# Optimization experiments

Hardware: AMD Instinct MI355X
Metric: run time of the kernel (lower is better)

Reference implementation:

```python
import jax, jax.numpy as jnp
import numpy as np

# Mamba2 derived dims (headdim=64, ngroups=1, mamba_ssm defaults)
D_MODEL = 1024
D_STATE = 64
D_CONV = 4
EXPAND = 2
D_INNER = EXPAND * D_MODEL          # 2048
HEADDIM = 64
NHEADS = D_INNER // HEADDIM          # 32
CONV_DIM = D_INNER + 2 * D_STATE     # 2176 (x, B, C share the depthwise conv)
D_IN_PROJ = 2 * D_INNER + 2 * D_STATE + NHEADS  # 4256 (z, xBC, dt)
BATCH, SEQ = 8, 1024


def setup_inputs() -> dict:
    key = jax.random.key(0)
    ks = jax.random.split(key, 8)
    g = lambda k, shp, sc=0.02: (jax.random.normal(k, shp, jnp.float32) * sc)
    # dt_bias init as in mamba_ssm: inverse-softplus of dt ~ U[1e-3, 1e-1] (log-uniform)
    dt = jnp.exp(jax.random.uniform(ks[3], (NHEADS,), jnp.float32)
                 * (jnp.log(0.1) - jnp.log(0.001)) + jnp.log(0.001))
    dt_bias = dt + jnp.log(-jnp.expm1(-dt))  # softplus^{-1}(dt)
    A_log = jnp.log(jax.random.uniform(ks[4], (NHEADS,), jnp.float32, 1.0, 16.0))
    return {
        "x": jax.random.normal(ks[0], (BATCH, SEQ, D_MODEL), jnp.float32),
        "W_in": g(ks[1], (D_MODEL, D_IN_PROJ)),
        "conv_w": g(ks[2], (D_CONV, CONV_DIM), 0.2),
        "conv_b": jnp.zeros((CONV_DIM,), jnp.float32),
        "dt_bias": dt_bias,
        "A_log": A_log,
        "Dskip": jnp.ones((NHEADS,), jnp.float32),
        "norm_w": jnp.ones((D_INNER,), jnp.float32),
        "W_out": g(ks[5], (D_INNER, D_MODEL)),
        "head_w": g(ks[6], (D_MODEL, 1)),
        "head_b": jnp.zeros((1,), jnp.float32),
    }


def _mamba2(x, W_in, conv_w, conv_b, dt_bias, A_log, Dskip, norm_w, W_out):
    b, l, _ = x.shape
    zxbcdt = x @ W_in                                   # (b, l, 4256)
    z = zxbcdt[..., :D_INNER]
    xBC = zxbcdt[..., D_INNER:D_INNER + CONV_DIM]
    dt = jax.nn.softplus(zxbcdt[..., D_INNER + CONV_DIM:] + dt_bias)  # (b, l, h)
    # causal depthwise conv1d (kernel D_CONV) + SiLU
    pad = jnp.pad(xBC, ((0, 0), (D_CONV - 1, 0), (0, 0)))
    conv = conv_b + sum(pad[:, k:k + l, :] * conv_w[k] for k in range(D_CONV))
    xBC = jax.nn.silu(conv)
    xh = xBC[..., :D_INNER].reshape(b, l, NHEADS, HEADDIM)
    B = xBC[..., D_INNER:D_INNER + D_STATE]             # (b, l, s) ngroups=1
    C = xBC[..., D_INNER + D_STATE:]                    # (b, l, s)
    A = -jnp.exp(A_log)                                 # (h,)
    dA = jnp.exp(dt * A)                                # (b, l, h)

    def step(h, inps):
        dA_t, dt_t, B_t, C_t, x_t = inps                # (b,h),(b,h),(b,s),(b,s),(b,h,p)
        h = h * dA_t[:, :, None, None] + (dt_t[:, :, None] * x_t)[..., None] * B_t[:, None, None, :]
        y = jnp.einsum('bhps,bs->bhp', h, C_t)
        return h, y

    tm = lambda a: jnp.moveaxis(a, 1, 0)                # time-major for scan
    h0 = jnp.zeros((b, NHEADS, HEADDIM, D_STATE), x.dtype)
    _, y = jax.lax.scan(step, h0, (tm(dA), tm(dt), tm(B), tm(C), tm(xh)))
    y = jnp.moveaxis(y, 0, 1) + Dskip[None, None, :, None] * xh   # skip connection
    # gated RMSNorm: norm(y * silu(z)) * weight
    y = y.reshape(b, l, D_INNER) * jax.nn.silu(z)
    y = y * jax.lax.rsqrt(jnp.mean(y * y, axis=-1, keepdims=True) + 1e-5) * norm_w
    return y @ W_out                                    # (b, l, d_model)


def reference(x, W_in, conv_w, conv_b, dt_bias, A_log, Dskip, norm_w, W_out, head_w, head_b):
    y = _mamba2(x, W_in, conv_w, conv_b, dt_bias, A_log, Dskip, norm_w, W_out)
    return y @ head_w + head_b                          # (b, l, 1)
```

## Files before the change

### kernel.cpp

```cpp
#include <hip/hip_runtime.h>
#include <hip/hip_bf16.h>

#define D_MODEL   1024
#define D_STATE   64
#define D_INNER   2048
#define NHEADS    32
#define CONV_DIM  2176
#define D_IN_PROJ 4256
#define NPAD      4352
#define BATCH     8
#define SEQ       1024
#define NROWS     8192
#define NCHUNK    8
#define CLEN      128

typedef __attribute__((ext_vector_type(8))) short bf16x8;
typedef __attribute__((ext_vector_type(4))) float f32x4;

__device__ __forceinline__ float bf2f(unsigned short u){
  unsigned v = ((unsigned)u) << 16;
  return __builtin_bit_cast(float, v);
}
__device__ __forceinline__ unsigned short f2bf(float f){
  __hip_bfloat16 h = __float2bfloat16(f);
  return __builtin_bit_cast(unsigned short, h);
}

__global__ __launch_bounds__(256) void k_convert_x(const float* __restrict__ x,
                                                   unsigned short* __restrict__ xb){
  int i = blockIdx.x*256 + threadIdx.x;
  float4 v = ((const float4*)x)[i];
  ushort4 o;
  o.x = f2bf(v.x); o.y = f2bf(v.y); o.z = f2bf(v.z); o.w = f2bf(v.w);
  ((ushort4*)xb)[i] = o;
}

__global__ __launch_bounds__(256) void k_transpose_win(const float* __restrict__ W_in,
                                                       unsigned short* __restrict__ wt){
  __shared__ float tile[32][33];
  int n0 = blockIdx.x * 32;
  int k0 = blockIdx.y * 32;
  int tx = threadIdx.x & 31;
  int ty = threadIdx.x >> 5;
  #pragma unroll
  for (int i = 0; i < 4; ++i){
    int kk = ty + i*8;
    int n  = n0 + tx;
    tile[kk][tx] = (n < D_IN_PROJ) ? W_in[(size_t)(k0+kk)*D_IN_PROJ + n] : 0.f;
  }
  __syncthreads();
  #pragma unroll
  for (int i = 0; i < 4; ++i){
    int nn = ty + i*8;
    wt[(size_t)(n0+nn)*D_MODEL + k0 + tx] = f2bf(tile[tx][nn]);
  }
}

__global__ __launch_bounds__(256) void k_nwc(const float* __restrict__ W_out,
                                             const float* __restrict__ head_w,
                                             const float* __restrict__ norm_w,
                                             float* __restrict__ nwc){
  int d    = blockIdx.x*4 + (threadIdx.x >> 6);
  int lane = threadIdx.x & 63;
  const float* row = W_out + (size_t)d * D_MODEL;
  float s = 0.f;
  #pragma unroll
  for (int k = lane; k < D_MODEL; k += 64) s += row[k] * head_w[k];
  #pragma unroll
  for (int off = 32; off; off >>= 1) s += __shfl_down(s, off);
  if (lane == 0) nwc[d] = s * norm_w[d];
}

__global__ __launch_bounds__(512, 1) void k_gemm256(const unsigned short* __restrict__ A,
                                                    const unsigned short* __restrict__ BT,
                                                    unsigned short* __restrict__ C){
  __shared__ unsigned short smem[65536];
  int bid  = blockIdx.x;
  int m0   = (bid / 17) << 8;
  int n0   = (bid % 17) << 8;
  int tid  = threadIdx.x;
  int w    = tid >> 6, lane = tid & 63;
  int wr   = w >> 2, wc = w & 3;
  int stR  = tid >> 3;
  int stC  = (tid & 7) << 3;
  int wb   = w << 9;

  f32x4 acc[8][4];
  #pragma unroll
  for (int i = 0; i < 8; ++i)
    #pragma unroll
    for (int j = 0; j < 4; ++j) acc[i][j] = (f32x4){0.f,0.f,0.f,0.f};

  const unsigned short* sA0 = A  + (size_t)(m0 + stR)*D_MODEL + stC;
  const unsigned short* sB0 = BT + (size_t)(n0 + stR)*D_MODEL + stC;

#define STAGE256(bb, kt) { \
    const unsigned short* pa = sA0 + (size_t)(kt)*64; \
    const unsigned short* pb = sB0 + (size_t)(kt)*64; \
    _Pragma("unroll") \
    for (int it = 0; it < 4; ++it){ \
      __builtin_amdgcn_global_load_lds((const __attribute__((address_space(1))) void*)(pa + (size_t)it*64*D_MODEL), \
          (__attribute__((address_space(3))) void*)(smem + (bb)*32768 + it*4096 + wb), 16, 0, 0); \
      __builtin_amdgcn_global_load_lds((const __attribute__((address_space(1))) void*)(pb + (size_t)it*64*D_MODEL), \
          (__attribute__((address_space(3))) void*)(smem + (bb)*32768 + 16384 + it*4096 + wb), 16, 0, 0); \
    } }

  STAGE256(0, 0);

  int frow = lane & 15, fk = (lane >> 4) << 3;

  for (int t = 0; t < 16; ++t){
    int cur = t & 1;
    asm volatile("" ::: "memory");
    __builtin_amdgcn_s_barrier();
    if (t < 15){
      STAGE256(cur ^ 1, t + 1);
      asm volatile("s_waitcnt vmcnt(8)" ::: "memory");
    } else {
      asm volatile("s_waitcnt vmcnt(0)" ::: "memory");
    }
    __builtin_amdgcn_s_barrier();
    asm volatile("" ::: "memory");

    const unsigned short* At = smem + cur*32768;
    const unsigned short* Bt = At + 16384;
    __builtin_amdgcn_s_setprio(1);
    #pragma unroll
    for (int kk = 0; kk < 64; kk += 32){
      bf16x8 af[8], bfr[4];
      #pragma unroll
      for (int mf = 0; mf < 8; ++mf)
        af[mf] = *(const bf16x8*)(At + (wr*128 + mf*16 + frow)*64 + kk + fk);
      #pragma unroll
      for (int nf = 0; nf < 4; ++nf)
        bfr[nf] = *(const bf16x8*)(Bt + (wc*64 + nf*16 + frow)*64 + kk + fk);
      #pragma unroll
      for (int mf = 0; mf < 8; ++mf)
        #pragma unroll
        for (int nf = 0; nf < 4; ++nf)
          acc[mf][nf] = __builtin_amdgcn_mfma_f32_16x16x32_bf16(af[mf], bfr[nf], acc[mf][nf], 0, 0, 0);
    }
    __builtin_amdgcn_s_setprio(0);
  }
#undef STAGE256

  int crow = (lane >> 4) << 2, ccol = lane & 15;
  #pragma unroll
  for (int mf = 0; mf < 8; ++mf)
    #pragma unroll
    for (int nf = 0; nf < 4; ++nf){
      size_t base = (size_t)(m0 + wr*128 + mf*16 + crow)*NPAD + (n0 + wc*64 + nf*16 + ccol);
      #pragma unroll
      for (int r = 0; r < 4; ++r)
        C[base + (size_t)r*NPAD] = f2bf(acc[mf][nf][r]);
    }
}

__global__ __launch_bounds__(256) void k_dtda(const unsigned short* __restrict__ zx,
                                              const float* __restrict__ dt_bias,
                                              float* __restrict__ dtb){
  int i = blockIdx.x*256 + threadIdx.x;
  int r = i >> 5, h = i & 31;
  float raw = bf2f(zx[(size_t)r*NPAD + D_INNER + CONV_DIM + h]) + dt_bias[h];
  float dt  = (raw > 20.f) ? raw : log1pf(expf(raw));
  int b = r >> 10, l = r & 1023;
  dtb[(b*32 + h)*1024 + l] = dt;
}

__global__ __launch_bounds__(256) void k_conv(const unsigned short* __restrict__ zx,
                                              const float* __restrict__ conv_w,
                                              const float* __restrict__ conv_b,
                                              unsigned short* __restrict__ xbc,
                                              unsigned short* __restrict__ bc16){
  int r = blockIdx.x;
  int l = r & (SEQ - 1);
  for (int oc = threadIdx.x; oc < 272; oc += 256){
    int c = oc * 8;
    float acc[8];
    #pragma unroll
    for (int j = 0; j < 8; ++j) acc[j] = conv_b[c + j];
    #pragma unroll
    for (int k = 0; k < 4; ++k){
      int dl = l + k - 3;
      if (dl >= 0){
        bf16x8 v = *(const bf16x8*)(zx + (size_t)(r + k - 3)*NPAD + D_INNER + c);
        #pragma unroll
        for (int j = 0; j < 8; ++j)
          acc[j] = fmaf(bf2f((unsigned short)v[j]), conv_w[k*CONV_DIM + c + j], acc[j]);
      }
    }
    bf16x8 o;
    #pragma unroll
    for (int j = 0; j < 8; ++j){
      float s = acc[j] / (1.f + expf(-acc[j]));
      o[j] = (short)f2bf(s);
    }
    if (c < D_INNER) *(bf16x8*)(xbc  + (size_t)r*D_INNER + c) = o;
    else             *(bf16x8*)(bc16 + (size_t)r*128 + (c - D_INNER)) = o;
  }
}

__global__ __launch_bounds__(64) void k_cs(const float* __restrict__ dtb,
                                           const float* __restrict__ A_log,
                                           float* __restrict__ csb,
                                           float* __restrict__ cumA){
  int id = blockIdx.x;
  int bh = id >> 3, c = id & 7;
  int h  = bh & 31;
  int l  = threadIdx.x;
  const float* src = dtb + (size_t)bh*1024 + (c << 7);
  float d0 = src[2*l], d1 = src[2*l + 1];
  float pr = d0 + d1;
  float s  = pr;
  #pragma unroll
  for (int off = 1; off < 64; off <<= 1){
    float n = __shfl_up(s, off);
    if (l >= off) s += n;
  }
  float excl = s - pr;
  csb[(size_t)id*128 + 2*l]     = excl + d0;
  csb[(size_t)id*128 + 2*l + 1] = excl + pr;
  if (l == 63){
    float A = -expf(A_log[h]);
    cumA[id] = expf(A * s);
  }
}

__global__ __launch_bounds__(256) void k_ssd1(const unsigned short* __restrict__ xbc,
                                              const unsigned short* __restrict__ bc16,
                                              const float* __restrict__ dtb,
                                              const float* __restrict__ csb,
                                              const float* __restrict__ A_log,
                                              unsigned short* __restrict__ hend){
  __shared__ __align__(16) unsigned short XTw[64*136];
  __shared__ __align__(16) unsigned short BTl[64*136];
  int id = blockIdx.x;
  int bh = id >> 3, c = id & 7;
  int b  = bh >> 5, h = bh & 31;
  int tid = threadIdx.x;
  int w = tid >> 6, l = tid & 63;
  float A = -expf(A_log[h]);
  int row0 = b*SEQ + (c << 7);
  float csT = csb[(size_t)id*128 + 127];

  #pragma unroll
  for (int it = 0; it < 4; ++it){
    int idx = it*256 + tid;
    int tau = idx >> 3, pb = idx & 7;
    bf16x8 v = *(const bf16x8*)(xbc + (size_t)(row0+tau)*D_INNER + h*64 + pb*8);
    float wgt = dtb[(size_t)bh*1024 + (c<<7) + tau]
              * expf(A*(csT - csb[(size_t)id*128 + tau]));
    #pragma unroll
    for (int j = 0; j < 8; ++j)
      XTw[(pb*8+j)*136 + tau] = f2bf(bf2f((unsigned short)v[j]) * wgt);
  }
  #pragma unroll
  for (int it = 0; it < 4; ++it){
    int idx = it*256 + tid;
    int tau = idx >> 3, sb = idx & 7;
    bf16x8 v = *(const bf16x8*)(bc16 + (size_t)(row0+tau)*128 + sb*8);
    #pragma unroll
    for (int j = 0; j < 8; ++j)
      BTl[(sb*8+j)*136 + tau] = (unsigned short)v[j];
  }
  __syncthreads();

  int fr = l & 15, fo = (l >> 4) << 3;
  f32x4 acc[4];
  #pragma unroll
  for (int n = 0; n < 4; ++n) acc[n] = (f32x4){0.f,0.f,0.f,0.f};
  #pragma unroll
  for (int kt = 0; kt < 4; ++kt){
    bf16x8 pf = *(const bf16x8*)(XTw + (w*16+fr)*136 + kt*32 + fo);
    #pragma unroll
    for (int n = 0; n < 4; ++n){
      bf16x8 qf = *(const bf16x8*)(BTl + (n*16+fr)*136 + kt*32 + fo);
      acc[n] = __builtin_amdgcn_mfma_f32_16x16x32_bf16(pf, qf, acc[n], 0, 0, 0);
    }
  }
  #pragma unroll
  for (int n = 0; n < 4; ++n)
    #pragma unroll
    for (int r = 0; r < 4; ++r){
      int p = w*16 + ((l>>4)<<2) + r;
      int s = n*16 + fr;
      hend[(size_t)id*4096 + p*64 + s] = f2bf(acc[n][r]);
    }
}

__global__ __launch_bounds__(256) void k_comb(unsigned short* __restrict__ hh,
                                              const float* __restrict__ cumA){
  int bh = blockIdx.x, tid = threadIdx.x;
  float carry[16];
  #pragma unroll
  for (int i = 0; i < 16; ++i) carry[i] = 0.f;
  #pragma unroll
  for (int c = 0; c < NCHUNK; ++c){
    size_t base = (((size_t)bh*NCHUNK + c) << 12) + tid*16;
    bf16x8 a0 = *(const bf16x8*)(hh + base);
    bf16x8 a1 = *(const bf16x8*)(hh + base + 8);
    float ca = cumA[bh*NCHUNK + c];
    float tmp[16];
    #pragma unroll
    for (int i = 0; i < 8; ++i){
      tmp[i]   = bf2f((unsigned short)a0[i]);
      tmp[8+i] = bf2f((unsigned short)a1[i]);
    }
    bf16x8 w0, w1;
    #pragma unroll
    for (int i = 0; i < 8; ++i){
      w0[i] = (short)f2bf(carry[i]);
      w1[i] = (short)f2bf(carry[8+i]);
    }
    *(bf16x8*)(hh + base)     = w0;
    *(bf16x8*)(hh + base + 8) = w1;
    #pragma unroll
    for (int i = 0; i < 16; ++i) carry[i] = tmp[i] + ca*carry[i];
  }
}

__global__ __launch_bounds__(256, 2) void k_ssd2(const unsigned short* __restrict__ xbc,
                                                 const unsigned short* __restrict__ bc16,
                                                 const unsigned short* __restrict__ zx,
                                                 const float* __restrict__ dtb,
                                                 const float* __restrict__ csb,
                                                 const float* __restrict__ A_log,
                                                 const float* __restrict__ Dskip,
                                                 const unsigned short* __restrict__ hbuf,
                                                 unsigned short* __restrict__ yb){
  __shared__ __align__(16) unsigned short Cl[128*72];
  __shared__ __align__(16) unsigned short XTl[64*136];
  __shared__ __align__(16) unsigned short Gm[128*136];
  __shared__ float cs_l[128], dt_l[128], a_l[128];

  int id = blockIdx.x;
  int bh = id >> 3, c = id & 7;
  int b  = bh >> 5, h = bh & 31;
  int tid = threadIdx.x;
  int w = tid >> 6, l = tid & 63;
  float A = -expf(A_log[h]);
  int row0 = b*SEQ + (c << 7);

  #pragma unroll
  for (int it = 0; it < 4; ++it){
    int idx = it*256 + tid;
    int tau = idx >> 3, cb = idx & 7;
    bf16x8 v = *(const bf16x8*)(bc16 + (size_t)(row0+tau)*128 + 64 + cb*8);
    *(bf16x8*)(Cl + tau*72 + cb*8) = v;
  }
  #pragma unroll
  for (int it = 0; it < 4; ++it){
    int idx = it*256 + tid;
    int tau = idx >> 3, pb = idx & 7;
    bf16x8 v = *(const bf16x8*)(xbc + (size_t)(row0+tau)*D_INNER + h*64 + pb*8);
    #pragma unroll
    for (int j = 0; j < 8; ++j)
      XTl[(pb*8+j)*136 + tau] = (unsigned short)v[j];
  }
  if (tid < 128){
    float cs = csb[(size_t)id*128 + tid];
    cs_l[tid] = cs;
    dt_l[tid] = dtb[(size_t)bh*1024 + (c<<7) + tid];
    a_l[tid]  = expf(A*cs);
  }
  __syncthreads();

  int fr = l & 15, fo = (l >> 4) << 3;
  int mtB = 7 - w;

  f32x4 Y[2][4];
  #pragma unroll
  for (int mi = 0; mi < 2; ++mi)
    #pragma unroll
    for (int n = 0; n < 4; ++n) Y[mi][n] = (f32x4){0.f,0.f,0.f,0.f};
  #pragma unroll
  for (int mi = 0; mi < 2; ++mi){
    int mt = mi ? mtB : w;
    #pragma unroll
    for (int kt = 0; kt < 2; ++kt){
      bf16x8 pf = *(const bf16x8*)(Cl + (mt*16+fr)*72 + kt*32 + fo);
      #pragma unroll
      for (int n = 0; n < 4; ++n){
        bf16x8 qf = *(const bf16x8*)(hbuf + (size_t)id*4096 + (n*16+fr)*64 + kt*32 + fo);
        Y[mi][n] = __builtin_amdgcn_mfma_f32_16x16x32_bf16(pf, qf, Y[mi][n], 0, 0, 0);
      }
    }
    #pragma unroll
    for (int r = 0; r < 4; ++r){
      float av = a_l[mt*16 + ((l>>4)<<2) + r];
      #pragma unroll
      for (int n = 0; n < 4; ++n) Y[mi][n][r] *= av;
    }
  }

  f32x4 Sv[9];
  #pragma unroll
  for (int slot = 0; slot < 9; ++slot){
    int mt = (slot <= w) ? w : mtB;
    int nt = (slot <= w) ? slot : slot - w - 1;
    f32x4 acc = (f32x4){0.f,0.f,0.f,0.f};
    #pragma unroll
    for (int kt = 0; kt < 2; ++kt){
      bf16x8 pf = *(const bf16x8*)(Cl + (mt*16+fr)*72 + kt*32 + fo);
      bf16x8 qf = *(const bf16x8*)(bc16 + (size_t)(row0 + nt*16+fr)*128 + kt*32 + fo);
      acc = __builtin_amdgcn_mfma_f32_16x16x32_bf16(pf, qf, acc, 0, 0, 0);
    }
    int tau = nt*16 + fr;
    float dtt = dt_l[tau];
    float cst = cs_l[tau];
    #pragma unroll
    for (int r = 0; r < 4; ++r){
      int t = mt*16 + ((l>>4)<<2) + r;
      float v = acc[r] * dtt * expf(A*(cs_l[t] - cst));
      acc[r] = (tau <= t) ? v : 0.f;
    }
    Sv[slot] = acc;
  }

  #pragma unroll
  for (int slot = 0; slot < 9; ++slot){
    int mt = (slot <= w) ? w : mtB;
    int nt = (slot <= w) ? slot : slot - w - 1;
    int tau = nt*16 + fr;
    #pragma unroll
    for (int r = 0; r < 4; ++r){
      int t = mt*16 + ((l>>4)<<2) + r;
      Gm[t*136 + tau] = f2bf(Sv[slot][r]);
    }
  }
  {
    int mtE = (w & 1) ? mtB : w;
    int ntE = mtE + 1;
    #pragma unroll
    for (int r = 0; r < 4; ++r){
      int t = mtE*16 + ((l>>4)<<2) + r;
      Gm[t*136 + ntE*16 + fr] = 0;
    }
  }
  __syncthreads();

  #pragma unroll
  for (int mi = 0; mi < 2; ++mi){
    int mt = mi ? mtB : w;
    int kmax = (mt + 2) >> 1;
    for (int kt2 = 0; kt2 < kmax; ++kt2){
      bf16x8 pf = *(const bf16x8*)(Gm + (mt*16+fr)*136 + kt2*32 + fo);
      #pragma unroll
      for (int n = 0; n < 4; ++n){
        bf16x8 qf = *(const bf16x8*)(XTl + (n*16+fr)*136 + kt2*32 + fo);
        Y[mi][n] = __builtin_amdgcn_mfma_f32_16x16x32_bf16(pf, qf, Y[mi][n], 0, 0, 0);
      }
    }
  }

  float dsk = Dskip[h];
  #pragma unroll
  for (int mi = 0; mi < 2; ++mi){
    int mt = mi ? mtB : w;
    #pragma unroll
    for (int r = 0; r < 4; ++r){
      int t = mt*16 + ((l>>4)<<2) + r;
      size_t orow = (size_t)(row0 + t)*D_INNER + h*64;
      size_t zrow = (size_t)(row0 + t)*NPAD + h*64;
      #pragma unroll
      for (int n = 0; n < 4; ++n){
        int p = n*16 + fr;
        float xv = bf2f(XTl[p*136 + t]);
        float zf = bf2f(zx[zrow + p]);
        float yv = Y[mi][n][r] + dsk*xv;
        float g  = yv * (zf / (1.f + expf(-zf)));
        yb[orow + p] = f2bf(g);
      }
    }
  }
}

__global__ __launch_bounds__(256) void k_epilogue(const unsigned short* __restrict__ yg,
                                                  const float* __restrict__ nwc,
                                                  const float* __restrict__ head_b,
                                                  float* __restrict__ out){
  int r   = blockIdx.x;
  int tid = threadIdx.x;
  bf16x8 y8 = *(const bf16x8*)(yg + (size_t)r*D_INNER + tid*8);
  float4 w0 = ((const float4*)nwc)[tid*2];
  float4 w1 = ((const float4*)nwc)[tid*2 + 1];
  float wv[8] = {w0.x, w0.y, w0.z, w0.w, w1.x, w1.y, w1.z, w1.w};
  float s2 = 0.f, sd = 0.f;
  #pragma unroll
  for (int k = 0; k < 8; ++k){
    float g = bf2f((unsigned short)y8[k]);
    s2 += g*g; sd += g*wv[k];
  }
  #pragma unroll
  for (int off = 32; off; off >>= 1){
    s2 += __shfl_down(s2, off);
    sd += __shfl_down(sd, off);
  }
  __shared__ float r2[4], rd[4];
  if ((tid & 63) == 0){ r2[tid >> 6] = s2; rd[tid >> 6] = sd; }
  __syncthreads();
  if (tid == 0){
    float t2 = r2[0] + r2[1] + r2[2] + r2[3];
    float td = rd[0] + rd[1] + rd[2] + rd[3];
    out[r] = rsqrtf(t2 * (1.f/2048.f) + 1e-5f) * td + head_b[0];
  }
}

extern "C" void kernel_launch(void* const* d_in, const int* in_sizes, int n_in,
                              void* d_out, int out_size, void* d_ws, size_t ws_size,
                              hipStream_t stream){
  const float* x       = (const float*)d_in[0];
  const float* W_in    = (const float*)d_in[1];
  const float* conv_w  = (const float*)d_in[2];
  const float* conv_b  = (const float*)d_in[3];
  const float* dt_bias = (const float*)d_in[4];
  const float* A_log   = (const float*)d_in[5];
  const float* Dskip   = (const float*)d_in[6];
  const float* norm_w  = (const float*)d_in[7];
  const float* W_out   = (const float*)d_in[8];
  const float* head_w  = (const float*)d_in[9];
  const float* head_b  = (const float*)d_in[10];
  float* out = (float*)d_out;

  char* ws = (char*)d_ws;
  unsigned short* xb   = (unsigned short*)(ws + 0);
  unsigned short* wt   = (unsigned short*)(ws + 16777216);
  unsigned short* zx16 = (unsigned short*)(ws + 25690112);
  unsigned short* xbc  = (unsigned short*)(ws + 96993280);
  float*          dtb  = (float*)         (ws + 132644864);
  float*          nwc  = (float*)         (ws + 134742016);
  unsigned short* yb   = (unsigned short*)(ws + 134750208);

  unsigned short* hbuf = xb;
  unsigned short* bc16 = wt;
  float*          csb  = (float*)(ws + 16777216 + 2097152);
  float*          cumA = (float*)(ws + 16777216 + 3145728);

  k_convert_x<<<8192, 256, 0, stream>>>(x, xb);
  k_transpose_win<<<dim3(136, 32), 256, 0, stream>>>(W_in, wt);
  k_nwc<<<512, 256, 0, stream>>>(W_out, head_w, norm_w, nwc);
  k_gemm256<<<(NROWS/256)*(NPAD/256), 512, 0, stream>>>(xb, wt, zx16);
  k_dtda<<<1024, 256, 0, stream>>>(zx16, dt_bias, dtb);
  k_conv<<<NROWS, 256, 0, stream>>>(zx16, conv_w, conv_b, xbc, bc16);
  k_cs<<<2048, 64, 0, stream>>>(dtb, A_log, csb, cumA);
  k_ssd1<<<2048, 256, 0, stream>>>(xbc, bc16, dtb, csb, A_log, hbuf);
  k_comb<<<256, 256, 0, stream>>>(hbuf, cumA);
  k_ssd2<<<2048, 256, 0, stream>>>(xbc, bc16, zx16, dtb, csb, A_log, Dskip, hbuf, yb);
  k_epilogue<<<NROWS, 256, 0, stream>>>(yb, nwc, head_b, out);
}
```

Baseline: 274.4 us.

## XOR-swizzle LDS tiles and interleave global-to-LDS loads with MFMA phases

The in-projection GEMM now XOR-swizzles the k-column placement of each row in LDS, applied on the global source address and undone on fragment reads, to cut LDS bank conflicts. The main loop is split into four sub-phases, and the next tile's B and A global_load_lds issues are spread between them with finer vmcnt waits and barriers. The aim is to overlap memory traffic with MFMA work rather than staging a whole tile up front. The risks are a hand-tuned vmcnt and barrier ordering that must exactly match when each buffer region is read, plus extra barriers per iteration.

```diff
diff --git a/kernel.cpp b/kernel.cpp
--- a/kernel.cpp
+++ b/kernel.cpp
@@ -82,8 +82,9 @@
   int w    = tid >> 6, lane = tid & 63;
   int wr   = w >> 2, wc = w & 3;
   int stR  = tid >> 3;
-  int stC  = (tid & 7) << 3;
+  int stCs = (((tid & 7) ^ ((tid >> 3) & 7)) << 3);
   int wb   = w << 9;
+  int frow = lane & 15, fk = (lane >> 4) << 3;
 
   f32x4 acc[8][4];
   #pragma unroll
@@ -91,58 +92,126 @@
     #pragma unroll
     for (int j = 0; j < 4; ++j) acc[i][j] = (f32x4){0.f,0.f,0.f,0.f};
 
-  const unsigned short* sA0 = A  + (size_t)(m0 + stR)*D_MODEL + stC;
-  const unsigned short* sB0 = BT + (size_t)(n0 + stR)*D_MODEL + stC;
-
-#define STAGE256(bb, kt) { \
-    const unsigned short* pa = sA0 + (size_t)(kt)*64; \
-    const unsigned short* pb = sB0 + (size_t)(kt)*64; \
-    _Pragma("unroll") \
-    for (int it = 0; it < 4; ++it){ \
-      __builtin_amdgcn_global_load_lds((const __attribute__((address_space(1))) void*)(pa + (size_t)it*64*D_MODEL), \
-          (__attribute__((address_space(3))) void*)(smem + (bb)*32768 + it*4096 + wb), 16, 0, 0); \
-      __builtin_amdgcn_global_load_lds((const __attribute__((address_space(1))) void*)(pb + (size_t)it*64*D_MODEL), \
-          (__attribute__((address_space(3))) void*)(smem + (bb)*32768 + 16384 + it*4096 + wb), 16, 0, 0); \
-    } }
-
-  STAGE256(0, 0);
-
-  int frow = lane & 15, fk = (lane >> 4) << 3;
+  const unsigned short* sA0 = A  + (size_t)(m0 + stR)*D_MODEL + stCs;
+  const unsigned short* sB0 = BT + (size_t)(n0 + stR)*D_MODEL + stCs;
+
+#define GLD(dstOff, src) __builtin_amdgcn_global_load_lds( \
+    (const __attribute__((address_space(1))) void*)(src), \
+    (__attribute__((address_space(3))) void*)(smem + (dstOff) + wb), 16, 0, 0)
+#define ISSA(bb,kt,i) GLD((bb)*32768 + (i)*4096, \
+    sA0 + (size_t)(kt)*64 + (size_t)(i)*64*D_MODEL)
+#define ISSB(bb,kt,i) GLD((bb)*32768 + 16384 + (i)*4096, \
+    sB0 + (size_t)(kt)*64 + (size_t)(i)*64*D_MODEL)
+#define RD8(base, r, col) (*(const bf16x8*)((base) + (r)*64 + ((col) ^ (((r)&7)<<3))))
+
+  ISSB(0,0,0); ISSB(0,0,1); ISSB(0,0,2); ISSB(0,0,3);
+  ISSA(0,0,0); ISSA(0,0,2); ISSA(0,0,1); ISSA(0,0,3);
+  asm volatile("s_waitcnt vmcnt(2)" ::: "memory");
+  __builtin_amdgcn_s_barrier();
+  asm volatile("" ::: "memory");
 
   for (int t = 0; t < 16; ++t){
-    int cur = t & 1;
-    asm volatile("" ::: "memory");
-    __builtin_amdgcn_s_barrier();
-    if (t < 15){
-      STAGE256(cur ^ 1, t + 1);
-      asm volatile("s_waitcnt vmcnt(8)" ::: "memory");
-    } else {
-      asm volatile("s_waitcnt vmcnt(0)" ::: "memory");
-    }
+    int cur = t & 1, nxt = cur ^ 1;
+    bool iss = (t < 15);
+    const unsigned short* At = smem + cur*32768;
+    const unsigned short* Bt = At + 16384;
+
+    bf16x8 bF[4][2];
+    if (iss){ ISSB(nxt, t+1, 0); ISSB(nxt, t+1, 1); }
+    #pragma unroll
+    for (int nf = 0; nf < 4; ++nf){
+      int r = wc*64 + nf*16 + frow;
+      bF[nf][0] = RD8(Bt, r, fk);
+      bF[nf][1] = RD8(Bt, r, 32 + fk);
+    }
+    {
+      bf16x8 aF[2][2];
+      #pragma unroll
+      for (int mi = 0; mi < 2; ++mi){
+        int r = wr*128 + mi*16 + frow;
+        aF[mi][0] = RD8(At, r, fk);
+        aF[mi][1] = RD8(At, r, 32 + fk);
+      }
+      __builtin_amdgcn_s_setprio(1);
+      #pragma unroll
+      for (int mi = 0; mi < 2; ++mi)
+        #pragma unroll
+        for (int nf = 0; nf < 4; ++nf)
+          #pragma unroll
+          for (int kki = 0; kki < 2; ++kki)
+            acc[mi][nf] = __builtin_amdgcn_mfma_f32_16x16x32_bf16(aF[mi][kki], bF[nf][kki], acc[mi][nf], 0, 0, 0);
+      __builtin_amdgcn_s_setprio(0);
+    }
+    if (iss){ ISSB(nxt, t+1, 2); ISSB(nxt, t+1, 3); }
+    {
+      bf16x8 aF[2][2];
+      #pragma unroll
+      for (int mi = 0; mi < 2; ++mi){
+        int r = wr*128 + (2 + mi)*16 + frow;
+        aF[mi][0] = RD8(At, r, fk);
+        aF[mi][1] = RD8(At, r, 32 + fk);
+      }
+      __builtin_amdgcn_s_setprio(1);
+      #pragma unroll
+      for (int mi = 0; mi < 2; ++mi)
+        #pragma unroll
+        for (int nf = 0; nf < 4; ++nf)
+          #pragma unroll
+          for (int kki = 0; kki < 2; ++kki)
+            acc[2 + mi][nf] = __builtin_amdgcn_mfma_f32_16x16x32_bf16(aF[mi][kki], bF[nf][kki], acc[2 + mi][nf], 0, 0, 0);
+      __builtin_amdgcn_s_setprio(0);
+    }
+    if (iss) asm volatile("s_waitcnt vmcnt(4)" ::: "memory");
+    else     asm volatile("s_waitcnt vmcnt(0)" ::: "memory");
     __builtin_amdgcn_s_barrier();
     asm volatile("" ::: "memory");
-
-    const unsigned short* At = smem + cur*32768;
-    const unsigned short* Bt = At + 16384;
-    __builtin_amdgcn_s_setprio(1);
-    #pragma unroll
-    for (int kk = 0; kk < 64; kk += 32){
-      bf16x8 af[8], bfr[4];
-      #pragma unroll
-      for (int mf = 0; mf < 8; ++mf)
-        af[mf] = *(const bf16x8*)(At + (wr*128 + mf*16 + frow)*64 + kk + fk);
-      #pragma unroll
-      for (int nf = 0; nf < 4; ++nf)
-        bfr[nf] = *(const bf16x8*)(Bt + (wc*64 + nf*16 + frow)*64 + kk + fk);
-      #pragma unroll
-      for (int mf = 0; mf < 8; ++mf)
+    if (iss){ ISSA(nxt, t+1, 0); ISSA(nxt, t+1, 2); }
+    {
+      bf16x8 aF[2][2];
+      #pragma unroll
+      for (int mi = 0; mi < 2; ++mi){
+        int r = wr*128 + (4 + mi)*16 + frow;
+        aF[mi][0] = RD8(At, r, fk);
+        aF[mi][1] = RD8(At, r, 32 + fk);
+      }
+      __builtin_amdgcn_s_setprio(1);
+      #pragma unroll
+      for (int mi = 0; mi < 2; ++mi)
         #pragma unroll
         for (int nf = 0; nf < 4; ++nf)
-          acc[mf][nf] = __builtin_amdgcn_mfma_f32_16x16x32_bf16(af[mf], bfr[nf], acc[mf][nf], 0, 0, 0);
-    }
-    __builtin_amdgcn_s_setprio(0);
-  }
-#undef STAGE256
+          #pragma unroll
+          for (int kki = 0; kki < 2; ++kki)
+            acc[4 + mi][nf] = __builtin_amdgcn_mfma_f32_16x16x32_bf16(aF[mi][kki], bF[nf][kki], acc[4 + mi][nf], 0, 0, 0);
+      __builtin_amdgcn_s_setprio(0);
+    }
+    if (iss){ ISSA(nxt, t+1, 1); ISSA(nxt, t+1, 3); }
+    {
+      bf16x8 aF[2][2];
+      #pragma unroll
+      for (int mi = 0; mi < 2; ++mi){
+        int r = wr*128 + (6 + mi)*16 + frow;
+        aF[mi][0] = RD8(At, r, fk);
+        aF[mi][1] = RD8(At, r, 32 + fk);
+      }
+      __builtin_amdgcn_s_setprio(1);
+      #pragma unroll
+      for (int mi = 0; mi < 2; ++mi)
+        #pragma unroll
+        for (int nf = 0; nf < 4; ++nf)
+          #pragma unroll
+          for (int kki = 0; kki < 2; ++kki)
+            acc[6 + mi][nf] = __builtin_amdgcn_mfma_f32_16x16x32_bf16(aF[mi][kki], bF[nf][kki], acc[6 + mi][nf], 0, 0, 0);
+      __builtin_amdgcn_s_setprio(0);
+    }
+    if (iss) asm volatile("s_waitcnt vmcnt(2)" ::: "memory");
+    else     asm volatile("s_waitcnt vmcnt(0)" ::: "memory");
+    __builtin_amdgcn_s_barrier();
+    asm volatile("" ::: "memory");
+  }
+#undef GLD
+#undef ISSA
+#undef ISSB
+#undef RD8
 
   int crow = (lane >> 4) << 2, ccol = lane & 15;
   #pragma unroll
```

Measured after the change: 246.5 us. 10.2% less time.

## Restructure in-projection GEMM into quarter phases with swizzled LDS and tile remap

Applied to the files above, without the earlier changes.

The 256x256 bf16 GEMM main loop is split into four quarter phases, each reading only part of the fragments from LDS. The next k-tile's global-to-LDS loads are spread across these phases with finer vmcnt waits, so memory traffic overlaps more evenly with MFMA work. LDS rows are XOR-swizzled on both store and read to cut bank conflicts, and block IDs are remapped for better L2 locality. In exchange the loop carries more barriers per k-step, and the tighter wait counts and swizzle indexing must stay exactly consistent.

```diff
diff --git a/kernel.cpp b/kernel.cpp
--- a/kernel.cpp
+++ b/kernel.cpp
@@ -76,14 +76,16 @@
                                                     unsigned short* __restrict__ C){
   __shared__ unsigned short smem[65536];
   int bid  = blockIdx.x;
-  int m0   = (bid / 17) << 8;
-  int n0   = (bid % 17) << 8;
+  int lt   = (bid & 7) * 68 + (bid >> 3);
+  int m0   = (lt / 17) << 8;
+  int n0   = (lt % 17) << 8;
   int tid  = threadIdx.x;
   int w    = tid >> 6, lane = tid & 63;
   int wr   = w >> 2, wc = w & 3;
   int stR  = tid >> 3;
-  int stC  = (tid & 7) << 3;
+  int stCs = (((tid & 7) ^ ((tid >> 3) & 7)) << 3);
   int wb   = w << 9;
+  int frow = lane & 15, fk = (lane >> 4) << 3;
 
   f32x4 acc[8][4];
   #pragma unroll
@@ -91,58 +93,80 @@
     #pragma unroll
     for (int j = 0; j < 4; ++j) acc[i][j] = (f32x4){0.f,0.f,0.f,0.f};
 
-  const unsigned short* sA0 = A  + (size_t)(m0 + stR)*D_MODEL + stC;
-  const unsigned short* sB0 = BT + (size_t)(n0 + stR)*D_MODEL + stC;
-
-#define STAGE256(bb, kt) { \
-    const unsigned short* pa = sA0 + (size_t)(kt)*64; \
-    const unsigned short* pb = sB0 + (size_t)(kt)*64; \
-    _Pragma("unroll") \
-    for (int it = 0; it < 4; ++it){ \
-      __builtin_amdgcn_global_load_lds((const __attribute__((address_space(1))) void*)(pa + (size_t)it*64*D_MODEL), \
-          (__attribute__((address_space(3))) void*)(smem + (bb)*32768 + it*4096 + wb), 16, 0, 0); \
-      __builtin_amdgcn_global_load_lds((const __attribute__((address_space(1))) void*)(pb + (size_t)it*64*D_MODEL), \
-          (__attribute__((address_space(3))) void*)(smem + (bb)*32768 + 16384 + it*4096 + wb), 16, 0, 0); \
-    } }
-
-  STAGE256(0, 0);
-
-  int frow = lane & 15, fk = (lane >> 4) << 3;
+  const unsigned short* sA0 = A  + (size_t)(m0 + stR)*D_MODEL + stCs;
+  const unsigned short* sB0 = BT + (size_t)(n0 + stR)*D_MODEL + stCs;
+
+#define GLD(dstOff, src) __builtin_amdgcn_global_load_lds( \
+    (const __attribute__((address_space(1))) void*)(src), \
+    (__attribute__((address_space(3))) void*)(smem + (dstOff) + wb), 16, 0, 0)
+#define ISSA(bb,kt,i) GLD((bb)*32768 + (i)*4096, \
+    sA0 + (size_t)(kt)*64 + (size_t)(i)*64*D_MODEL)
+#define ISSB(bb,kt,i) GLD((bb)*32768 + 16384 + (i)*4096, \
+    sB0 + (size_t)(kt)*64 + (size_t)(i)*64*D_MODEL)
+#define RD8(base, r, col) (*(const bf16x8*)((base) + (r)*64 + ((col) ^ (((r)&7)<<3))))
+
+  ISSB(0,0,0); ISSB(0,0,1); ISSB(0,0,2); ISSB(0,0,3);
+  ISSA(0,0,0); ISSA(0,0,2); ISSA(0,0,1); ISSA(0,0,3);
+  asm volatile("s_waitcnt vmcnt(2)" ::: "memory");
+  __builtin_amdgcn_s_barrier();
+  asm volatile("" ::: "memory");
 
   for (int t = 0; t < 16; ++t){
-    int cur = t & 1;
-    asm volatile("" ::: "memory");
-    __builtin_amdgcn_s_barrier();
-    if (t < 15){
-      STAGE256(cur ^ 1, t + 1);
-      asm volatile("s_waitcnt vmcnt(8)" ::: "memory");
-    } else {
-      asm volatile("s_waitcnt vmcnt(0)" ::: "memory");
-    }
-    __builtin_amdgcn_s_barrier();
-    asm volatile("" ::: "memory");
-
+    int cur = t & 1, nxt = cur ^ 1;
+    bool iss = (t < 15);
     const unsigned short* At = smem + cur*32768;
     const unsigned short* Bt = At + 16384;
-    __builtin_amdgcn_s_setprio(1);
-    #pragma unroll
-    for (int kk = 0; kk < 64; kk += 32){
-      bf16x8 af[8], bfr[4];
-      #pragma unroll
-      for (int mf = 0; mf < 8; ++mf)
-        af[mf] = *(const bf16x8*)(At + (wr*128 + mf*16 + frow)*64 + kk + fk);
-      #pragma unroll
-      for (int nf = 0; nf < 4; ++nf)
-        bfr[nf] = *(const bf16x8*)(Bt + (wc*64 + nf*16 + frow)*64 + kk + fk);
-      #pragma unroll
-      for (int mf = 0; mf < 8; ++mf)
-        #pragma unroll
-        for (int nf = 0; nf < 4; ++nf)
-          acc[mf][nf] = __builtin_amdgcn_mfma_f32_16x16x32_bf16(af[mf], bfr[nf], acc[mf][nf], 0, 0, 0);
-    }
-    __builtin_amdgcn_s_setprio(0);
-  }
-#undef STAGE256
+
+#define QPHASE(mh, nh, ISSUE_STMT, WAIT_STMT) { \
+    bf16x8 aF[4][2], bQ[2][2]; \
+    _Pragma("unroll") \
+    for (int mi = 0; mi < 4; ++mi){ \
+      int r = wr*128 + (mh)*64 + mi*16 + frow; \
+      aF[mi][0] = RD8(At, r, fk); \
+      aF[mi][1] = RD8(At, r, 32 + fk); \
+    } \
+    _Pragma("unroll") \
+    for (int ni = 0; ni < 2; ++ni){ \
+      int r = wc*64 + (nh)*32 + ni*16 + frow; \
+      bQ[ni][0] = RD8(Bt, r, fk); \
+      bQ[ni][1] = RD8(Bt, r, 32 + fk); \
+    } \
+    ISSUE_STMT; \
+    asm volatile("" ::: "memory"); \
+    __builtin_amdgcn_s_barrier(); \
+    asm volatile("" ::: "memory"); \
+    __builtin_amdgcn_s_setprio(1); \
+    _Pragma("unroll") \
+    for (int mi = 0; mi < 4; ++mi) \
+      _Pragma("unroll") \
+      for (int ni = 0; ni < 2; ++ni) \
+        _Pragma("unroll") \
+        for (int kki = 0; kki < 2; ++kki) \
+          acc[(mh)*4+mi][(nh)*2+ni] = __builtin_amdgcn_mfma_f32_16x16x32_bf16( \
+              aF[mi][kki], bQ[ni][kki], acc[(mh)*4+mi][(nh)*2+ni], 0, 0, 0); \
+    __builtin_amdgcn_s_setprio(0); \
+    WAIT_STMT; \
+    asm volatile("" ::: "memory"); \
+    __builtin_amdgcn_s_barrier(); \
+    asm volatile("" ::: "memory"); }
+
+    QPHASE(0, 0,
+      if (iss){ ISSB(nxt, t+1, 0); ISSB(nxt, t+1, 1); }, )
+    QPHASE(0, 1,
+      if (iss){ ISSB(nxt, t+1, 2); ISSB(nxt, t+1, 3); },
+      if (iss) asm volatile("s_waitcnt vmcnt(4)" ::: "memory");
+      else     asm volatile("s_waitcnt vmcnt(0)" ::: "memory"); )
+    QPHASE(1, 0,
+      if (iss){ ISSA(nxt, t+1, 0); ISSA(nxt, t+1, 2); }, )
+    QPHASE(1, 1,
+      if (iss){ ISSA(nxt, t+1, 1); ISSA(nxt, t+1, 3); },
+      if (iss) asm volatile("s_waitcnt vmcnt(2)" ::: "memory"); )
+#undef QPHASE
+  }
+#undef GLD
+#undef ISSA
+#undef ISSB
+#undef RD8
 
   int crow = (lane >> 4) << 2, ccol = lane & 15;
   #pragma unroll
```

Measured after the change: 254.9 us. 1.08x faster.
